# Kernel optimization log

Measured on AMD Instinct MI355X. Metric: run time of the kernel, lower is better.

Reference implementation:

```python
import jax, jax.numpy as jnp
import numpy as np

DIM = 1024
EXP = 4
B, S = 4, 4096


def setup_inputs() -> dict:
    key = jax.random.key(0)
    ks = jax.random.split(key, 20)
    d, h = DIM, DIM * EXP
    sc = 1.0 / np.sqrt(d)
    inp = {
        "x": jax.random.normal(ks[0], (B, S, d), dtype=jnp.float32),
        # attention linears, stored [in, out] so y = x @ W + b
        "wq": jax.random.normal(ks[1], (d, d), jnp.float32) * sc,
        "bq": jnp.zeros((d,), jnp.float32),
        "wk": jax.random.normal(ks[2], (d, d), jnp.float32) * sc,
        "bk": jnp.zeros((d,), jnp.float32),
        "wv": jax.random.normal(ks[3], (d, d), jnp.float32) * sc,
        "bv": jnp.zeros((d,), jnp.float32),
        "wo": jax.random.normal(ks[4], (d, d), jnp.float32) * sc,
        "bo": jnp.zeros((d,), jnp.float32),
        # FFN
        "w1": jax.random.normal(ks[5], (d, h), jnp.float32) * sc,
        "b1": jnp.zeros((h,), jnp.float32),
        "w2": jax.random.normal(ks[6], (h, d), jnp.float32) * (1.0 / np.sqrt(h)),
        "b2": jnp.zeros((d,), jnp.float32),
        # LayerNorms
        "g1": jnp.ones((d,), jnp.float32),
        "beta1": jnp.zeros((d,), jnp.float32),
        "g2": jnp.ones((d,), jnp.float32),
        "beta2": jnp.zeros((d,), jnp.float32),
    }
    return inp


def _layernorm(x, g, b, eps=1e-5):
    mu = jnp.mean(x, axis=-1, keepdims=True)
    var = jnp.mean(jnp.square(x - mu), axis=-1, keepdims=True)
    return (x - mu) * jax.lax.rsqrt(var + eps) * g + b


def _block(x, wq, bq, wk, bk, wv, bv, wo, bo, w1, b1, w2, b2, g1, beta1, g2, beta2):
    d = x.shape[-1]
    # attention sub-block (single head, full [B,S,S] scores as in source)
    h = _layernorm(x, g1, beta1)
    q = h @ wq + bq
    k = h @ wk + bk
    v = h @ wv + bv
    scores = jnp.einsum("bsd,btd->bst", q, k) / jnp.sqrt(jnp.asarray(d, x.dtype))
    attn = jax.nn.softmax(scores, axis=-1)
    a = jnp.einsum("bst,btd->bsd", attn, v) @ wo + bo
    x = x + a
    # FFN sub-block (exact GELU, matching torch nn.GELU default)
    h2 = _layernorm(x, g2, beta2)
    f = jax.nn.gelu(h2 @ w1 + b1, approximate=False) @ w2 + b2
    return x + f


def reference(x, wq, bq, wk, bk, wv, bv, wo, bo, w1, b1, w2, b2, g1, beta1, g2, beta2):
    return _block(x, wq, bq, wk, bk, wv, bv, wo, bo, w1, b1, w2, b2, g1, beta1, g2, beta2)
```

## Files before the change

### kernel.cpp

```cpp
#include <hip/hip_runtime.h>
#include <hip/hip_bf16.h>
#include <cstdint>

typedef __bf16 bf16;
typedef __bf16 bf16x8 __attribute__((ext_vector_type(8)));
typedef __bf16 bf16x4 __attribute__((ext_vector_type(4)));
typedef float f32x4 __attribute__((ext_vector_type(4)));

#define DEV __device__ __forceinline__

DEV float wred_sum(float v) {
#pragma unroll
  for (int off = 32; off > 0; off >>= 1) v += __shfl_xor(v, off, 64);
  return v;
}
DEV float wred_max(float v) {
#pragma unroll
  for (int off = 32; off > 0; off >>= 1) v = fmaxf(v, __shfl_xor(v, off, 64));
  return v;
}

__global__ void convT_kernel(const float* __restrict__ in, bf16* __restrict__ out,
                             int K, int N) {
  __shared__ float t[32][33];
  const int n0 = blockIdx.x * 32, k0 = blockIdx.y * 32;
  const int tx = threadIdx.x & 31, ty = threadIdx.x >> 5;
#pragma unroll
  for (int i = 0; i < 4; i++)
    t[ty + 8 * i][tx] = in[(long)(k0 + ty + 8 * i) * N + n0 + tx];
  __syncthreads();
#pragma unroll
  for (int i = 0; i < 4; i++)
    out[(long)(n0 + ty + 8 * i) * K + k0 + tx] = (bf16)t[tx][ty + 8 * i];
}

__global__ void transpose_bf16(const bf16* __restrict__ in, bf16* __restrict__ out,
                               int ldin, int ldout) {
  __shared__ bf16 t[32][33];
  const int c0 = blockIdx.x * 32, r0 = blockIdx.y * 32;
  const int tx = threadIdx.x & 31, ty = threadIdx.x >> 5;
#pragma unroll
  for (int i = 0; i < 4; i++)
    t[ty + 8 * i][tx] = in[(long)(r0 + ty + 8 * i) * ldin + c0 + tx];
  __syncthreads();
#pragma unroll
  for (int i = 0; i < 4; i++)
    out[(long)(c0 + ty + 8 * i) * ldout + r0 + tx] = t[tx][ty + 8 * i];
}

__global__ void ln_bf16_kernel(const float* __restrict__ x, const float* __restrict__ g,
                               const float* __restrict__ be, bf16* __restrict__ out) {
  const long row = blockIdx.x;
  const int tid = threadIdx.x;
  const float4 v = ((const float4*)(x + row * 1024))[tid];
  float s = v.x + v.y + v.z + v.w;
  float s2 = v.x * v.x + v.y * v.y + v.z * v.z + v.w * v.w;
  __shared__ float rs_[4], rs2_[4];
  s = wred_sum(s);
  s2 = wred_sum(s2);
  const int wave = tid >> 6, lane = tid & 63;
  if (lane == 0) { rs_[wave] = s; rs2_[wave] = s2; }
  __syncthreads();
  s = rs_[0] + rs_[1] + rs_[2] + rs_[3];
  s2 = rs2_[0] + rs2_[1] + rs2_[2] + rs2_[3];
  const float mu = s * (1.0f / 1024.0f);
  const float var = s2 * (1.0f / 1024.0f) - mu * mu;
  const float rstd = rsqrtf(var + 1e-5f);
  const float4 gg = ((const float4*)g)[tid];
  const float4 bb = ((const float4*)be)[tid];
  bf16x4 o;
  o[0] = (bf16)((v.x - mu) * rstd * gg.x + bb.x);
  o[1] = (bf16)((v.y - mu) * rstd * gg.y + bb.y);
  o[2] = (bf16)((v.z - mu) * rstd * gg.z + bb.z);
  o[3] = (bf16)((v.w - mu) * rstd * gg.w + bb.w);
  *(bf16x4*)(out + row * 1024 + tid * 4) = o;
}

__global__ void softmax_kernel(bf16* __restrict__ p) {
  const long row = blockIdx.x;
  bf16* pr = p + row * 4096;
  const int tid = threadIdx.x;
  bf16x8 a = *(const bf16x8*)(pr + tid * 16);
  bf16x8 b = *(const bf16x8*)(pr + tid * 16 + 8);
  float v[16];
#pragma unroll
  for (int i = 0; i < 8; i++) { v[i] = (float)a[i]; v[8 + i] = (float)b[i]; }
  float mx = -1e30f;
#pragma unroll
  for (int i = 0; i < 16; i++) mx = fmaxf(mx, v[i]);
  __shared__ float red1[4], red2[4];
  mx = wred_max(mx);
  const int wave = tid >> 6, lane = tid & 63;
  if (lane == 0) red1[wave] = mx;
  __syncthreads();
  mx = fmaxf(fmaxf(red1[0], red1[1]), fmaxf(red1[2], red1[3]));
  float s = 0.0f;
#pragma unroll
  for (int i = 0; i < 16; i++) { v[i] = __expf(v[i] - mx); s += v[i]; }
  s = wred_sum(s);
  if (lane == 0) red2[wave] = s;
  __syncthreads();
  s = red2[0] + red2[1] + red2[2] + red2[3];
  const float inv = 1.0f / s;
#pragma unroll
  for (int i = 0; i < 8; i++) { a[i] = (bf16)(v[i] * inv); b[i] = (bf16)(v[8 + i] * inv); }
  *(bf16x8*)(pr + tid * 16) = a;
  *(bf16x8*)(pr + tid * 16 + 8) = b;
}

enum { EPI_BF16 = 0, EPI_QKV = 1, EPI_GELU = 2, EPI_F32RES = 3 };

DEV void stage16(const bf16* g, bf16* l) {
  __builtin_amdgcn_global_load_lds((const __attribute__((address_space(1))) void*)g,
                                   (__attribute__((address_space(3))) void*)l, 16, 0, 0);
}

template <int EPI>
__global__ __launch_bounds__(256, 2)
void gemm128(const bf16* __restrict__ A, const bf16* __restrict__ B,
             const float* __restrict__ bias, const float* __restrict__ resid,
             void* Cout, int M, int N, int K,
             int lda, int ldb, int ldc, float alpha) {
  __shared__ __align__(16) bf16 sA[2 * 8192];
  __shared__ __align__(16) bf16 sB[2 * 8192];
  const int tid = threadIdx.x;
  const int lane = tid & 63;
  const int wid = tid >> 6;
  const int q = lane >> 4, r16 = lane & 15;
  const int wr = wid >> 1, wc = wid & 1;
  const long m0 = (long)blockIdx.y * 128;
  const long n0 = (long)blockIdx.x * 128;
  const int srow = tid >> 3;
  const int gcol = ((tid & 7) ^ (srow & 7)) * 8;
  const long lda32 = (long)lda * 32, ldb32 = (long)ldb * 32;
  const bf16* Ag = A + (m0 + srow) * (long)lda + gcol;
  const bf16* Bg = B + (n0 + srow) * (long)ldb + gcol;
  const int NT = K >> 6;
  const int swz = r16 * 64 + ((q ^ (r16 & 7)) * 8);
  const int abase = wr * 4096 + swz;
  const int bbase = wc * 4096 + swz;
  f32x4 acc[4][4] = {};

#pragma unroll
  for (int blk = 0; blk < 4; ++blk) {
    stage16(Ag + blk * lda32, sA + tid * 8 + blk * 2048);
    stage16(Bg + blk * ldb32, sB + tid * 8 + blk * 2048);
  }
  asm volatile("s_waitcnt vmcnt(0)" ::: "memory");
  __builtin_amdgcn_sched_barrier(0);
  __builtin_amdgcn_s_barrier();
  __builtin_amdgcn_sched_barrier(0);

  for (int t = 0; t < NT; ++t) {
    const int bx = (t & 1) * 8192;
    const int nbx = 8192 - bx;
    if (t + 1 < NT) {
      const bf16* Agn = Ag + (t + 1) * 64;
      const bf16* Bgn = Bg + (t + 1) * 64;
#pragma unroll
      for (int blk = 0; blk < 4; ++blk) {
        stage16(Agn + blk * lda32, sA + nbx + tid * 8 + blk * 2048);
        stage16(Bgn + blk * ldb32, sB + nbx + tid * 8 + blk * 2048);
      }
    }
    const bf16* sAb = sA + bx;
    const bf16* sBb = sB + bx;
    bf16x8 a0[4], a1[4], b0[4], b1[4];
#pragma unroll
    for (int i = 0; i < 4; ++i) {
      a0[i] = *(const bf16x8*)(sAb + (abase + i * 1024));
      a1[i] = *(const bf16x8*)(sAb + ((abase + i * 1024) ^ 32));
      b0[i] = *(const bf16x8*)(sBb + (bbase + i * 1024));
      b1[i] = *(const bf16x8*)(sBb + ((bbase + i * 1024) ^ 32));
    }
#pragma unroll
    for (int i = 0; i < 4; ++i)
#pragma unroll
      for (int j = 0; j < 4; ++j) {
        acc[i][j] = __builtin_amdgcn_mfma_f32_16x16x32_bf16(b0[j], a0[i], acc[i][j], 0, 0, 0);
        acc[i][j] = __builtin_amdgcn_mfma_f32_16x16x32_bf16(b1[j], a1[i], acc[i][j], 0, 0, 0);
      }
    if (t + 1 < NT) {
      asm volatile("s_waitcnt vmcnt(0)" ::: "memory");
      __builtin_amdgcn_sched_barrier(0);
      __builtin_amdgcn_s_barrier();
      __builtin_amdgcn_sched_barrier(0);
    }
  }

#pragma unroll
  for (int i = 0; i < 4; ++i) {
    const long row = m0 + wr * 64 + i * 16 + r16;
#pragma unroll
    for (int j = 0; j < 4; ++j) {
      const int ncol = (int)n0 + wc * 64 + j * 16 + q * 4;
      float4 b4 = make_float4(0.f, 0.f, 0.f, 0.f);
      if (bias != nullptr) b4 = *(const float4*)(bias + ncol);
      float v0 = acc[i][j][0] * alpha + b4.x;
      float v1 = acc[i][j][1] * alpha + b4.y;
      float v2 = acc[i][j][2] * alpha + b4.z;
      float v3 = acc[i][j][3] * alpha + b4.w;
      if (EPI == EPI_F32RES) {
        const long idx = row * (long)ldc + ncol;
        const float4 rr = *(const float4*)(resid + idx);
        const float4 o = make_float4(v0 + rr.x, v1 + rr.y, v2 + rr.z, v3 + rr.w);
        *(float4*)((float*)Cout + idx) = o;
      } else {
        bf16x4 o;
        o[0] = (bf16)v0; o[1] = (bf16)v1; o[2] = (bf16)v2; o[3] = (bf16)v3;
        *(bf16x4*)((bf16*)Cout + row * (long)ldc + ncol) = o;
      }
    }
  }
}

template <int EPI>
__global__ __launch_bounds__(512, 2)
void gemm256(const bf16* __restrict__ A, const bf16* __restrict__ B,
             const float* __restrict__ bias, const float* bias2, const float* bias3,
             const float* resid, void* Cout, int M, int N, int K,
             int lda, int ldb, int ldc, float alpha) {
  extern __shared__ __align__(16) char smem[];
  bf16* sA = (bf16*)smem;
  bf16* sB = sA + 32768;
  const int tid = threadIdx.x;
  const int lane = tid & 63;
  const int wid = tid >> 6;
  const int q = lane >> 4, r16 = lane & 15;
  const int wr = wid >> 2, wc = wid & 3;
  const long m0 = (long)blockIdx.y * 256;
  const long n0 = (long)blockIdx.x * 256;
  const int srow = tid >> 3;
  const int gcol = ((tid & 7) ^ (srow & 7)) * 8;
  const long lda64 = (long)lda * 64, ldb64 = (long)ldb * 64;
  const bf16* AgT = A + (m0 + srow) * (long)lda + gcol;
  const bf16* BgT = B + (n0 + srow) * (long)ldb + gcol;
  bf16* lA = sA + tid * 8;
  bf16* lB = sB + tid * 8;
  const int NT = K >> 6;
  const int swz = r16 * 64 + ((q ^ (r16 & 7)) * 8);
  const int abase = wr * 8192 + swz;
  const int bbase = (wc >> 1) * 8192 + (wc & 1) * 4096 + swz;

  f32x4 acc[8][4] = {};

  stage16(BgT,             lB);
  stage16(BgT + ldb64,     lB + 4096);
  stage16(BgT + 2 * ldb64, lB + 8192);
  stage16(BgT + 3 * ldb64, lB + 12288);
  stage16(AgT,             lA);
  stage16(AgT + lda64,     lA + 4096);
  stage16(AgT + 2 * lda64, lA + 8192);
  stage16(AgT + 3 * lda64, lA + 12288);
  if (NT > 1) {
    stage16(BgT + 64,             lB + 16384);
    stage16(BgT + 64 + ldb64,     lB + 16384 + 4096);
    stage16(BgT + 64 + 2 * ldb64, lB + 16384 + 8192);
    stage16(BgT + 64 + 3 * ldb64, lB + 16384 + 12288);
    asm volatile("s_waitcnt vmcnt(4)" ::: "memory");
  } else {
    asm volatile("s_waitcnt vmcnt(0)" ::: "memory");
  }
  __builtin_amdgcn_sched_barrier(0);
  __builtin_amdgcn_s_barrier();
  __builtin_amdgcn_sched_barrier(0);

  for (int t = 0; t < NT; ++t) {
    const int bx = (t & 1) * 16384;
    const int nbx = 16384 - bx;
    const bf16* sAb = sA + bx;
    const bf16* sBb = sB + bx;
    bf16x8 b0[4], b1[4];
#pragma unroll
    for (int p = 0; p < 4; ++p) {
      if (p == 0) {
#pragma unroll
        for (int n = 0; n < 4; ++n) {
          b0[n] = *(const bf16x8*)(sBb + (bbase + n * 1024));
          b1[n] = *(const bf16x8*)(sBb + ((bbase + n * 1024) ^ 32));
        }
      }
      const int ab = abase + p * 2048;
      const bf16x8 a00 = *(const bf16x8*)(sAb + ab);
      const bf16x8 a10 = *(const bf16x8*)(sAb + (ab ^ 32));
      const bf16x8 a01 = *(const bf16x8*)(sAb + (ab + 1024));
      const bf16x8 a11 = *(const bf16x8*)(sAb + ((ab + 1024) ^ 32));
      if (p == 0 && t + 1 < NT) {
        stage16(AgT + 64,         lA + nbx);
        stage16(AgT + 64 + lda64, lA + nbx + 4096);
      }
      if (p == 1 && t + 1 < NT) {
        stage16(AgT + 64 + 2 * lda64, lA + nbx + 8192);
        stage16(AgT + 64 + 3 * lda64, lA + nbx + 12288);
      }
      if (p == 2 && t + 2 < NT) {
        stage16(BgT + 128,         lB + bx);
        stage16(BgT + 128 + ldb64, lB + bx + 4096);
      }
      if (p == 3 && t + 2 < NT) {
        stage16(BgT + 128 + 2 * ldb64, lB + bx + 8192);
        stage16(BgT + 128 + 3 * ldb64, lB + bx + 12288);
      }
      __builtin_amdgcn_sched_barrier(0);
      __builtin_amdgcn_s_barrier();
      __builtin_amdgcn_sched_barrier(0);
      __builtin_amdgcn_s_setprio(1);
#pragma unroll
      for (int n = 0; n < 4; ++n) {
        acc[2 * p][n]     = __builtin_amdgcn_mfma_f32_16x16x32_bf16(b0[n], a00, acc[2 * p][n], 0, 0, 0);
        acc[2 * p][n]     = __builtin_amdgcn_mfma_f32_16x16x32_bf16(b1[n], a10, acc[2 * p][n], 0, 0, 0);
        acc[2 * p + 1][n] = __builtin_amdgcn_mfma_f32_16x16x32_bf16(b0[n], a01, acc[2 * p + 1][n], 0, 0, 0);
        acc[2 * p + 1][n] = __builtin_amdgcn_mfma_f32_16x16x32_bf16(b1[n], a11, acc[2 * p + 1][n], 0, 0, 0);
      }
      __builtin_amdgcn_s_setprio(0);
      if (p == 3) {
        if (t + 2 < NT)      asm volatile("s_waitcnt vmcnt(4)" ::: "memory");
        else if (t + 1 < NT) asm volatile("s_waitcnt vmcnt(0)" ::: "memory");
      }
      __builtin_amdgcn_sched_barrier(0);
      __builtin_amdgcn_s_barrier();
      __builtin_amdgcn_sched_barrier(0);
    }
    AgT += 64;
    BgT += 64;
  }

#pragma unroll
  for (int m = 0; m < 8; ++m) {
    const long row = m0 + wr * 128 + m * 16 + r16;
#pragma unroll
    for (int n = 0; n < 4; ++n) {
      const int ncol = (int)n0 + wc * 64 + n * 16 + q * 4;
      float4 b4 = make_float4(0.f, 0.f, 0.f, 0.f);
      if (EPI == EPI_QKV) {
        const int band = ncol >> 10;
        const float* bsel = band == 0 ? bias : (band == 1 ? bias2 : bias3);
        b4 = *(const float4*)(bsel + (ncol & 1023));
      } else if (bias != nullptr) {
        b4 = *(const float4*)(bias + ncol);
      }
      float v0 = acc[m][n][0] * alpha + b4.x;
      float v1 = acc[m][n][1] * alpha + b4.y;
      float v2 = acc[m][n][2] * alpha + b4.z;
      float v3 = acc[m][n][3] * alpha + b4.w;
      if (EPI == EPI_GELU) {
        v0 = 0.5f * v0 * (1.0f + erff(v0 * 0.70710678118654752f));
        v1 = 0.5f * v1 * (1.0f + erff(v1 * 0.70710678118654752f));
        v2 = 0.5f * v2 * (1.0f + erff(v2 * 0.70710678118654752f));
        v3 = 0.5f * v3 * (1.0f + erff(v3 * 0.70710678118654752f));
      }
      if (EPI == EPI_F32RES) {
        const long idx = row * (long)ldc + ncol;
        const float4 rr = *(const float4*)(resid + idx);
        const float4 o = make_float4(v0 + rr.x, v1 + rr.y, v2 + rr.z, v3 + rr.w);
        *(float4*)((float*)Cout + idx) = o;
      } else {
        bf16x4 o;
        o[0] = (bf16)v0; o[1] = (bf16)v1; o[2] = (bf16)v2; o[3] = (bf16)v3;
        *(bf16x4*)((bf16*)Cout + row * (long)ldc + ncol) = o;
      }
    }
  }
}

extern "C" void kernel_launch(void* const* d_in, const int* in_sizes, int n_in,
                              void* d_out, int out_size, void* d_ws, size_t ws_size,
                              hipStream_t stream) {
  const float* x  = (const float*)d_in[0];
  const float* wq = (const float*)d_in[1];
  const float* bq = (const float*)d_in[2];
  const float* wk = (const float*)d_in[3];
  const float* bk = (const float*)d_in[4];
  const float* wv = (const float*)d_in[5];
  const float* bv = (const float*)d_in[6];
  const float* wo = (const float*)d_in[7];
  const float* bo = (const float*)d_in[8];
  const float* w1 = (const float*)d_in[9];
  const float* b1 = (const float*)d_in[10];
  const float* w2 = (const float*)d_in[11];
  const float* b2 = (const float*)d_in[12];
  const float* g1 = (const float*)d_in[13];
  const float* be1 = (const float*)d_in[14];
  const float* g2 = (const float*)d_in[15];
  const float* be2 = (const float*)d_in[16];

  static int attr_done = 0;
  if (!attr_done) {
    attr_done = 1;
    hipFuncSetAttribute(reinterpret_cast<const void*>(&gemm256<EPI_QKV>),
                        hipFuncAttributeMaxDynamicSharedMemorySize, 131072);
    hipFuncSetAttribute(reinterpret_cast<const void*>(&gemm256<EPI_BF16>),
                        hipFuncAttributeMaxDynamicSharedMemorySize, 131072);
    hipFuncSetAttribute(reinterpret_cast<const void*>(&gemm256<EPI_GELU>),
                        hipFuncAttributeMaxDynamicSharedMemorySize, 131072);
    hipFuncSetAttribute(reinterpret_cast<const void*>(&gemm256<EPI_F32RES>),
                        hipFuncAttributeMaxDynamicSharedMemorySize, 131072);
  }

  const long MB = 1 << 20;
  char* ws = (char*)d_ws;
  char* ob = (char*)d_out;
  bf16* WQKV = (bf16*)(ws + 0 * MB);
  bf16* WO   = (bf16*)(ws + 6 * MB);
  bf16* W1   = (bf16*)(ws + 8 * MB);
  bf16* W2   = (bf16*)(ws + 16 * MB);
  bf16* H    = (bf16*)(ws + 24 * MB);
  bf16* P    = (bf16*)(ob + 0 * MB);
  bf16* QKVb = (bf16*)(ob + 32 * MB);
  bf16* Vt   = (bf16*)(ob + 56 * MB);
  float* OUT = (float*)d_out;
  const dim3 blk(256);
  const dim3 blk512(512);
  const size_t SMEM = 131072;

  convT_kernel<<<dim3(32, 32), blk, 0, stream>>>(wq, WQKV, 1024, 1024);
  convT_kernel<<<dim3(32, 32), blk, 0, stream>>>(wk, WQKV + 1024 * 1024, 1024, 1024);
  convT_kernel<<<dim3(32, 32), blk, 0, stream>>>(wv, WQKV + 2048 * 1024, 1024, 1024);
  convT_kernel<<<dim3(32, 32), blk, 0, stream>>>(wo, WO, 1024, 1024);
  convT_kernel<<<dim3(128, 32), blk, 0, stream>>>(w1, W1, 1024, 4096);
  convT_kernel<<<dim3(32, 128), blk, 0, stream>>>(w2, W2, 4096, 1024);
  ln_bf16_kernel<<<16384, blk, 0, stream>>>(x, g1, be1, H);
  for (int z = 0; z < 4; z++) {
    const long zo = (long)z * 4096 * 1024;
    gemm256<EPI_QKV><<<dim3(12, 16), blk512, SMEM, stream>>>(
        H + zo, WQKV, bq, bk, bv, nullptr, QKVb,
        4096, 3072, 1024, 1024, 1024, 3072, 1.0f);
    transpose_bf16<<<dim3(32, 128), blk, 0, stream>>>(QKVb + 2048, Vt, 3072, 4096);
    gemm256<EPI_BF16><<<dim3(16, 16), blk512, SMEM, stream>>>(
        QKVb, QKVb + 1024, nullptr, nullptr, nullptr, nullptr, P,
        4096, 4096, 1024, 3072, 3072, 4096, 1.0f / 32.0f);
    softmax_kernel<<<4096, blk, 0, stream>>>(P);
    gemm128<EPI_BF16><<<dim3(8, 32), blk, 0, stream>>>(
        P, Vt, nullptr, nullptr, H + zo,
        4096, 1024, 4096, 4096, 4096, 1024, 1.0f);
  }
  gemm256<EPI_F32RES><<<dim3(4, 64), blk512, SMEM, stream>>>(
      H, WO, bo, nullptr, nullptr, x, OUT,
      16384, 1024, 1024, 1024, 1024, 1024, 1.0f);
  bf16* H2m = (bf16*)(ws + 0 * MB);
  bf16* Fm  = (bf16*)(ws + 24 * MB);
  for (int mc = 0; mc < 4; mc++) {
    const long ro = (long)mc * 4096 * 1024;
    ln_bf16_kernel<<<4096, blk, 0, stream>>>(OUT + ro, g2, be2, H2m);
    gemm256<EPI_GELU><<<dim3(16, 16), blk512, SMEM, stream>>>(
        H2m, W1, b1, nullptr, nullptr, nullptr, Fm,
        4096, 4096, 1024, 1024, 1024, 4096, 1.0f);
    gemm128<EPI_F32RES><<<dim3(8, 32), blk, 0, stream>>>(
        Fm, W2, b2, OUT + ro, OUT + ro,
        4096, 1024, 4096, 4096, 4096, 1024, 1.0f);
  }
  (void)in_sizes; (void)n_in; (void)out_size; (void)ws_size;
}
```

Measured before the change: 1.439 ms.

## Replace 256-tile GEMMs with 128 tiles, add 64-row 3-stage GEMM and XCD swizzle

Removes the 256x256 512-thread GEMM and routes the QKV, scores, WO and FFN1 GEMMs through the 128x128 kernel, which gains QKV-bias and GELU epilogues. A new 64x128 GEMM with a three-stage LDS ring buffer handles the long-K P·V and FFN2 products. Both GEMMs remap block indices with an XCD-aware swizzle to improve L2 locality. Smaller tiles increase block counts and occupancy but lower per-block data reuse compared with the 256 tiles.

```diff
diff --git a/kernel.cpp b/kernel.cpp
--- a/kernel.cpp
+++ b/kernel.cpp
@@ -115,21 +115,30 @@
                                    (__attribute__((address_space(3))) void*)l, 16, 0, 0);
 }
 
+DEV int xcd_swizzle(int flat, int nwg) {
+  const int qq = nwg >> 3, rr = nwg & 7;
+  const int xcd = flat & 7, idx = flat >> 3;
+  return (xcd < rr ? xcd * (qq + 1) : rr * (qq + 1) + (xcd - rr) * qq) + idx;
+}
+
 template <int EPI>
 __global__ __launch_bounds__(256, 2)
 void gemm128(const bf16* __restrict__ A, const bf16* __restrict__ B,
-             const float* __restrict__ bias, const float* __restrict__ resid,
-             void* Cout, int M, int N, int K,
+             const float* __restrict__ bias, const float* bias2, const float* bias3,
+             const float* resid, void* Cout, int M, int N, int K,
              int lda, int ldb, int ldc, float alpha) {
   __shared__ __align__(16) bf16 sA[2 * 8192];
   __shared__ __align__(16) bf16 sB[2 * 8192];
+  int flat = (int)(blockIdx.y * gridDim.x + blockIdx.x);
+  flat = xcd_swizzle(flat, (int)(gridDim.x * gridDim.y));
+  const int bix = flat % (int)gridDim.x, biy = flat / (int)gridDim.x;
   const int tid = threadIdx.x;
   const int lane = tid & 63;
   const int wid = tid >> 6;
   const int q = lane >> 4, r16 = lane & 15;
   const int wr = wid >> 1, wc = wid & 1;
-  const long m0 = (long)blockIdx.y * 128;
-  const long n0 = (long)blockIdx.x * 128;
+  const long m0 = (long)biy * 128;
+  const long n0 = (long)bix * 128;
   const int srow = tid >> 3;
   const int gcol = ((tid & 7) ^ (srow & 7)) * 8;
   const long lda32 = (long)lda * 32, ldb32 = (long)ldb * 32;
@@ -195,11 +204,23 @@
     for (int j = 0; j < 4; ++j) {
       const int ncol = (int)n0 + wc * 64 + j * 16 + q * 4;
       float4 b4 = make_float4(0.f, 0.f, 0.f, 0.f);
-      if (bias != nullptr) b4 = *(const float4*)(bias + ncol);
+      if (EPI == EPI_QKV) {
+        const int band = ncol >> 10;
+        const float* bsel = band == 0 ? bias : (band == 1 ? bias2 : bias3);
+        b4 = *(const float4*)(bsel + (ncol & 1023));
+      } else if (bias != nullptr) {
+        b4 = *(const float4*)(bias + ncol);
+      }
       float v0 = acc[i][j][0] * alpha + b4.x;
       float v1 = acc[i][j][1] * alpha + b4.y;
       float v2 = acc[i][j][2] * alpha + b4.z;
       float v3 = acc[i][j][3] * alpha + b4.w;
+      if (EPI == EPI_GELU) {
+        v0 = 0.5f * v0 * (1.0f + erff(v0 * 0.70710678118654752f));
+        v1 = 0.5f * v1 * (1.0f + erff(v1 * 0.70710678118654752f));
+        v2 = 0.5f * v2 * (1.0f + erff(v2 * 0.70710678118654752f));
+        v3 = 0.5f * v3 * (1.0f + erff(v3 * 0.70710678118654752f));
+      }
       if (EPI == EPI_F32RES) {
         const long idx = row * (long)ldc + ncol;
         const float4 rr = *(const float4*)(resid + idx);
@@ -215,140 +236,108 @@
 }
 
 template <int EPI>
-__global__ __launch_bounds__(512, 2)
-void gemm256(const bf16* __restrict__ A, const bf16* __restrict__ B,
-             const float* __restrict__ bias, const float* bias2, const float* bias3,
-             const float* resid, void* Cout, int M, int N, int K,
-             int lda, int ldb, int ldc, float alpha) {
+__global__ __launch_bounds__(256, 2)
+void gemm64(const bf16* __restrict__ A, const bf16* __restrict__ B,
+            const float* __restrict__ bias, const float* __restrict__ resid,
+            void* Cout, int M, int N, int K,
+            int lda, int ldb, int ldc, float alpha) {
   extern __shared__ __align__(16) char smem[];
   bf16* sA = (bf16*)smem;
-  bf16* sB = sA + 32768;
+  bf16* sB = sA + 3 * 4096;
+  int flat = (int)(blockIdx.y * gridDim.x + blockIdx.x);
+  flat = xcd_swizzle(flat, (int)(gridDim.x * gridDim.y));
+  const int bix = flat % (int)gridDim.x, biy = flat / (int)gridDim.x;
   const int tid = threadIdx.x;
   const int lane = tid & 63;
   const int wid = tid >> 6;
   const int q = lane >> 4, r16 = lane & 15;
-  const int wr = wid >> 2, wc = wid & 3;
-  const long m0 = (long)blockIdx.y * 256;
-  const long n0 = (long)blockIdx.x * 256;
+  const int wr = wid >> 1, wc = wid & 1;
+  const long m0 = (long)biy * 64;
+  const long n0 = (long)bix * 128;
   const int srow = tid >> 3;
   const int gcol = ((tid & 7) ^ (srow & 7)) * 8;
-  const long lda64 = (long)lda * 64, ldb64 = (long)ldb * 64;
-  const bf16* AgT = A + (m0 + srow) * (long)lda + gcol;
-  const bf16* BgT = B + (n0 + srow) * (long)ldb + gcol;
-  bf16* lA = sA + tid * 8;
-  bf16* lB = sB + tid * 8;
+  const long lda32 = (long)lda * 32, ldb32 = (long)ldb * 32;
+  const bf16* Ag = A + (m0 + srow) * (long)lda + gcol;
+  const bf16* Bg = B + (n0 + srow) * (long)ldb + gcol;
   const int NT = K >> 6;
   const int swz = r16 * 64 + ((q ^ (r16 & 7)) * 8);
-  const int abase = wr * 8192 + swz;
-  const int bbase = (wc >> 1) * 8192 + (wc & 1) * 4096 + swz;
-
-  f32x4 acc[8][4] = {};
-
-  stage16(BgT,             lB);
-  stage16(BgT + ldb64,     lB + 4096);
-  stage16(BgT + 2 * ldb64, lB + 8192);
-  stage16(BgT + 3 * ldb64, lB + 12288);
-  stage16(AgT,             lA);
-  stage16(AgT + lda64,     lA + 4096);
-  stage16(AgT + 2 * lda64, lA + 8192);
-  stage16(AgT + 3 * lda64, lA + 12288);
-  if (NT > 1) {
-    stage16(BgT + 64,             lB + 16384);
-    stage16(BgT + 64 + ldb64,     lB + 16384 + 4096);
-    stage16(BgT + 64 + 2 * ldb64, lB + 16384 + 8192);
-    stage16(BgT + 64 + 3 * ldb64, lB + 16384 + 12288);
-    asm volatile("s_waitcnt vmcnt(4)" ::: "memory");
-  } else {
-    asm volatile("s_waitcnt vmcnt(0)" ::: "memory");
-  }
+  const int abase = wr * 2048 + swz;
+  const int bbase = wc * 4096 + swz;
+  f32x4 acc[2][4] = {};
+
+  const int PRE = NT < 2 ? NT : 2;
+  for (int tt = 0; tt < PRE; ++tt) {
+#pragma unroll
+    for (int blk = 0; blk < 2; ++blk)
+      stage16(Ag + tt * 64 + blk * lda32, sA + tt * 4096 + tid * 8 + blk * 2048);
+#pragma unroll
+    for (int blk = 0; blk < 4; ++blk)
+      stage16(Bg + tt * 64 + blk * ldb32, sB + tt * 8192 + tid * 8 + blk * 2048);
+  }
+  if (NT >= 2) asm volatile("s_waitcnt vmcnt(6)" ::: "memory");
+  else         asm volatile("s_waitcnt vmcnt(0)" ::: "memory");
   __builtin_amdgcn_sched_barrier(0);
   __builtin_amdgcn_s_barrier();
   __builtin_amdgcn_sched_barrier(0);
 
+  int bxA = 0, bxB = 0;
+  int bsA = 8192, bsB = 16384;
   for (int t = 0; t < NT; ++t) {
-    const int bx = (t & 1) * 16384;
-    const int nbx = 16384 - bx;
-    const bf16* sAb = sA + bx;
-    const bf16* sBb = sB + bx;
-    bf16x8 b0[4], b1[4];
-#pragma unroll
-    for (int p = 0; p < 4; ++p) {
-      if (p == 0) {
-#pragma unroll
-        for (int n = 0; n < 4; ++n) {
-          b0[n] = *(const bf16x8*)(sBb + (bbase + n * 1024));
-          b1[n] = *(const bf16x8*)(sBb + ((bbase + n * 1024) ^ 32));
-        }
-      }
-      const int ab = abase + p * 2048;
-      const bf16x8 a00 = *(const bf16x8*)(sAb + ab);
-      const bf16x8 a10 = *(const bf16x8*)(sAb + (ab ^ 32));
-      const bf16x8 a01 = *(const bf16x8*)(sAb + (ab + 1024));
-      const bf16x8 a11 = *(const bf16x8*)(sAb + ((ab + 1024) ^ 32));
-      if (p == 0 && t + 1 < NT) {
-        stage16(AgT + 64,         lA + nbx);
-        stage16(AgT + 64 + lda64, lA + nbx + 4096);
-      }
-      if (p == 1 && t + 1 < NT) {
-        stage16(AgT + 64 + 2 * lda64, lA + nbx + 8192);
-        stage16(AgT + 64 + 3 * lda64, lA + nbx + 12288);
-      }
-      if (p == 2 && t + 2 < NT) {
-        stage16(BgT + 128,         lB + bx);
-        stage16(BgT + 128 + ldb64, lB + bx + 4096);
-      }
-      if (p == 3 && t + 2 < NT) {
-        stage16(BgT + 128 + 2 * ldb64, lB + bx + 8192);
-        stage16(BgT + 128 + 3 * ldb64, lB + bx + 12288);
-      }
+    if (t + 2 < NT) {
+      const bf16* Agn = Ag + (t + 2) * 64;
+      const bf16* Bgn = Bg + (t + 2) * 64;
+#pragma unroll
+      for (int blk = 0; blk < 2; ++blk)
+        stage16(Agn + blk * lda32, sA + bsA + tid * 8 + blk * 2048);
+#pragma unroll
+      for (int blk = 0; blk < 4; ++blk)
+        stage16(Bgn + blk * ldb32, sB + bsB + tid * 8 + blk * 2048);
+    }
+    const bf16* sAb = sA + bxA;
+    const bf16* sBb = sB + bxB;
+    bf16x8 a0[2], a1[2], b0[4], b1[4];
+#pragma unroll
+    for (int i = 0; i < 2; ++i) {
+      a0[i] = *(const bf16x8*)(sAb + (abase + i * 1024));
+      a1[i] = *(const bf16x8*)(sAb + ((abase + i * 1024) ^ 32));
+    }
+#pragma unroll
+    for (int j = 0; j < 4; ++j) {
+      b0[j] = *(const bf16x8*)(sBb + (bbase + j * 1024));
+      b1[j] = *(const bf16x8*)(sBb + ((bbase + j * 1024) ^ 32));
+    }
+#pragma unroll
+    for (int i = 0; i < 2; ++i)
+#pragma unroll
+      for (int j = 0; j < 4; ++j) {
+        acc[i][j] = __builtin_amdgcn_mfma_f32_16x16x32_bf16(b0[j], a0[i], acc[i][j], 0, 0, 0);
+        acc[i][j] = __builtin_amdgcn_mfma_f32_16x16x32_bf16(b1[j], a1[i], acc[i][j], 0, 0, 0);
+      }
+    if (t + 2 < NT)      asm volatile("s_waitcnt vmcnt(6)" ::: "memory");
+    else if (t + 1 < NT) asm volatile("s_waitcnt vmcnt(0)" ::: "memory");
+    if (t + 1 < NT) {
       __builtin_amdgcn_sched_barrier(0);
       __builtin_amdgcn_s_barrier();
       __builtin_amdgcn_sched_barrier(0);
-      __builtin_amdgcn_s_setprio(1);
-#pragma unroll
-      for (int n = 0; n < 4; ++n) {
-        acc[2 * p][n]     = __builtin_amdgcn_mfma_f32_16x16x32_bf16(b0[n], a00, acc[2 * p][n], 0, 0, 0);
-        acc[2 * p][n]     = __builtin_amdgcn_mfma_f32_16x16x32_bf16(b1[n], a10, acc[2 * p][n], 0, 0, 0);
-        acc[2 * p + 1][n] = __builtin_amdgcn_mfma_f32_16x16x32_bf16(b0[n], a01, acc[2 * p + 1][n], 0, 0, 0);
-        acc[2 * p + 1][n] = __builtin_amdgcn_mfma_f32_16x16x32_bf16(b1[n], a11, acc[2 * p + 1][n], 0, 0, 0);
-      }
-      __builtin_amdgcn_s_setprio(0);
-      if (p == 3) {
-        if (t + 2 < NT)      asm volatile("s_waitcnt vmcnt(4)" ::: "memory");
-        else if (t + 1 < NT) asm volatile("s_waitcnt vmcnt(0)" ::: "memory");
-      }
-      __builtin_amdgcn_sched_barrier(0);
-      __builtin_amdgcn_s_barrier();
-      __builtin_amdgcn_sched_barrier(0);
-    }
-    AgT += 64;
-    BgT += 64;
-  }
-
-#pragma unroll
-  for (int m = 0; m < 8; ++m) {
-    const long row = m0 + wr * 128 + m * 16 + r16;
-#pragma unroll
-    for (int n = 0; n < 4; ++n) {
-      const int ncol = (int)n0 + wc * 64 + n * 16 + q * 4;
+    }
+    bxA += 4096; if (bxA == 12288) bxA = 0;
+    bxB += 8192; if (bxB == 24576) bxB = 0;
+    bsA += 4096; if (bsA == 12288) bsA = 0;
+    bsB += 8192; if (bsB == 24576) bsB = 0;
+  }
+
+#pragma unroll
+  for (int i = 0; i < 2; ++i) {
+    const long row = m0 + wr * 32 + i * 16 + r16;
+#pragma unroll
+    for (int j = 0; j < 4; ++j) {
+      const int ncol = (int)n0 + wc * 64 + j * 16 + q * 4;
       float4 b4 = make_float4(0.f, 0.f, 0.f, 0.f);
-      if (EPI == EPI_QKV) {
-        const int band = ncol >> 10;
-        const float* bsel = band == 0 ? bias : (band == 1 ? bias2 : bias3);
-        b4 = *(const float4*)(bsel + (ncol & 1023));
-      } else if (bias != nullptr) {
-        b4 = *(const float4*)(bias + ncol);
-      }
-      float v0 = acc[m][n][0] * alpha + b4.x;
-      float v1 = acc[m][n][1] * alpha + b4.y;
-      float v2 = acc[m][n][2] * alpha + b4.z;
-      float v3 = acc[m][n][3] * alpha + b4.w;
-      if (EPI == EPI_GELU) {
-        v0 = 0.5f * v0 * (1.0f + erff(v0 * 0.70710678118654752f));
-        v1 = 0.5f * v1 * (1.0f + erff(v1 * 0.70710678118654752f));
-        v2 = 0.5f * v2 * (1.0f + erff(v2 * 0.70710678118654752f));
-        v3 = 0.5f * v3 * (1.0f + erff(v3 * 0.70710678118654752f));
-      }
+      if (bias != nullptr) b4 = *(const float4*)(bias + ncol);
+      float v0 = acc[i][j][0] * alpha + b4.x;
+      float v1 = acc[i][j][1] * alpha + b4.y;
+      float v2 = acc[i][j][2] * alpha + b4.z;
+      float v3 = acc[i][j][3] * alpha + b4.w;
       if (EPI == EPI_F32RES) {
         const long idx = row * (long)ldc + ncol;
         const float4 rr = *(const float4*)(resid + idx);
@@ -387,14 +376,10 @@
   static int attr_done = 0;
   if (!attr_done) {
     attr_done = 1;
-    hipFuncSetAttribute(reinterpret_cast<const void*>(&gemm256<EPI_QKV>),
-                        hipFuncAttributeMaxDynamicSharedMemorySize, 131072);
-    hipFuncSetAttribute(reinterpret_cast<const void*>(&gemm256<EPI_BF16>),
-                        hipFuncAttributeMaxDynamicSharedMemorySize, 131072);
-    hipFuncSetAttribute(reinterpret_cast<const void*>(&gemm256<EPI_GELU>),
-                        hipFuncAttributeMaxDynamicSharedMemorySize, 131072);
-    hipFuncSetAttribute(reinterpret_cast<const void*>(&gemm256<EPI_F32RES>),
-                        hipFuncAttributeMaxDynamicSharedMemorySize, 131072);
+    hipFuncSetAttribute(reinterpret_cast<const void*>(&gemm64<EPI_BF16>),
+                        hipFuncAttributeMaxDynamicSharedMemorySize, 73728);
+    hipFuncSetAttribute(reinterpret_cast<const void*>(&gemm64<EPI_F32RES>),
+                        hipFuncAttributeMaxDynamicSharedMemorySize, 73728);
   }
 
   const long MB = 1 << 20;
@@ -410,8 +395,7 @@
   bf16* Vt   = (bf16*)(ob + 56 * MB);
   float* OUT = (float*)d_out;
   const dim3 blk(256);
-  const dim3 blk512(512);
-  const size_t SMEM = 131072;
+  const size_t SMEM64 = 73728;
 
   convT_kernel<<<dim3(32, 32), blk, 0, stream>>>(wq, WQKV, 1024, 1024);
   convT_kernel<<<dim3(32, 32), blk, 0, stream>>>(wk, WQKV + 1024 * 1024, 1024, 1024);
@@ -422,19 +406,19 @@
   ln_bf16_kernel<<<16384, blk, 0, stream>>>(x, g1, be1, H);
   for (int z = 0; z < 4; z++) {
     const long zo = (long)z * 4096 * 1024;
-    gemm256<EPI_QKV><<<dim3(12, 16), blk512, SMEM, stream>>>(
+    gemm128<EPI_QKV><<<dim3(24, 32), blk, 0, stream>>>(
         H + zo, WQKV, bq, bk, bv, nullptr, QKVb,
         4096, 3072, 1024, 1024, 1024, 3072, 1.0f);
     transpose_bf16<<<dim3(32, 128), blk, 0, stream>>>(QKVb + 2048, Vt, 3072, 4096);
-    gemm256<EPI_BF16><<<dim3(16, 16), blk512, SMEM, stream>>>(
+    gemm128<EPI_BF16><<<dim3(32, 32), blk, 0, stream>>>(
         QKVb, QKVb + 1024, nullptr, nullptr, nullptr, nullptr, P,
         4096, 4096, 1024, 3072, 3072, 4096, 1.0f / 32.0f);
     softmax_kernel<<<4096, blk, 0, stream>>>(P);
-    gemm128<EPI_BF16><<<dim3(8, 32), blk, 0, stream>>>(
+    gemm64<EPI_BF16><<<dim3(8, 64), blk, SMEM64, stream>>>(
         P, Vt, nullptr, nullptr, H + zo,
         4096, 1024, 4096, 4096, 4096, 1024, 1.0f);
   }
-  gemm256<EPI_F32RES><<<dim3(4, 64), blk512, SMEM, stream>>>(
+  gemm128<EPI_F32RES><<<dim3(8, 128), blk, 0, stream>>>(
       H, WO, bo, nullptr, nullptr, x, OUT,
       16384, 1024, 1024, 1024, 1024, 1024, 1.0f);
   bf16* H2m = (bf16*)(ws + 0 * MB);
@@ -442,10 +426,10 @@
   for (int mc = 0; mc < 4; mc++) {
     const long ro = (long)mc * 4096 * 1024;
     ln_bf16_kernel<<<4096, blk, 0, stream>>>(OUT + ro, g2, be2, H2m);
-    gemm256<EPI_GELU><<<dim3(16, 16), blk512, SMEM, stream>>>(
+    gemm128<EPI_GELU><<<dim3(32, 32), blk, 0, stream>>>(
         H2m, W1, b1, nullptr, nullptr, nullptr, Fm,
         4096, 4096, 1024, 1024, 1024, 4096, 1.0f);
-    gemm128<EPI_F32RES><<<dim3(8, 32), blk, 0, stream>>>(
+    gemm64<EPI_F32RES><<<dim3(8, 64), blk, SMEM64, stream>>>(
         Fm, W2, b2, OUT + ro, OUT + ro,
         4096, 1024, 4096, 4096, 4096, 1024, 1.0f);
   }
```

After: 1.331 ms. 1.08x faster.
